# Optimization experiments

Hardware: AMD Instinct MI355X
Metric: run time of the kernel (lower is better)

Reference implementation:

```python
import jax, jax.numpy as jnp
import numpy as np
import math

B, S, D = 2, 2048, 1024
H, KV, HD = 16, 4, 64
N_REP = H // KV
ROPE_THETA = 1.0e6


def _rope_tables(seq_len, head_dim, theta):
    inv_freq = 1.0 / (theta ** (np.arange(0, head_dim, 2, dtype=np.float32) / head_dim))
    t = np.arange(seq_len, dtype=np.float32)
    freqs = np.outer(t, inv_freq)                      # [S, HD/2]
    emb = np.concatenate([freqs, freqs], axis=-1)      # [S, HD]
    return jnp.asarray(np.cos(emb)), jnp.asarray(np.sin(emb))


def setup_inputs() -> dict:
    key = jax.random.key(0)
    ks = jax.random.split(key, 6)
    cos, sin = _rope_tables(S, HD, ROPE_THETA)
    scale = 0.02
    return {
        "x": jax.random.normal(ks[0], (B, S, D), dtype=jnp.float32),
        "cos": cos,
        "sin": sin,
        "Wq": jax.random.normal(ks[1], (D, H * HD), dtype=jnp.float32) * scale,
        "Wk": jax.random.normal(ks[2], (D, KV * HD), dtype=jnp.float32) * scale,
        "Wv": jax.random.normal(ks[3], (D, KV * HD), dtype=jnp.float32) * scale,
        "Wo": jax.random.normal(ks[4], (H * HD, D), dtype=jnp.float32) * scale,
    }


def _rotate_half(u):
    u1, u2 = u[..., : HD // 2], u[..., HD // 2 :]
    return jnp.concatenate([-u2, u1], axis=-1)


def reference(x, cos, sin, Wq, Wk, Wv, Wo):
    bsz, seq_len, _ = x.shape
    q = (x @ Wq).reshape(bsz, seq_len, H, HD)   # [B,S,H,HD]
    k = (x @ Wk).reshape(bsz, seq_len, KV, HD)  # [B,S,KV,HD]
    v = (x @ Wv).reshape(bsz, seq_len, KV, HD)

    # RoPE: cos/sin [S,HD] broadcast over batch and heads (unsqueeze_dim=1)
    c = cos[:seq_len][None, :, None, :]
    s = sin[:seq_len][None, :, None, :]
    q = q * c + _rotate_half(q) * s
    k = k * c + _rotate_half(k) * s

    # repeat_kv: expand KV heads groupwise to H heads
    k = jnp.repeat(k, N_REP, axis=2)  # [B,S,H,HD]
    v = jnp.repeat(v, N_REP, axis=2)

    q = q.transpose(0, 2, 1, 3)  # [B,H,S,HD]
    k = k.transpose(0, 2, 1, 3)
    v = v.transpose(0, 2, 1, 3)

    scores = jnp.einsum("bhqd,bhkd->bhqk", q, k) / math.sqrt(HD)
    causal = jnp.tril(jnp.ones((seq_len, seq_len), dtype=bool))
    scores = jnp.where(causal[None, None], scores, jnp.finfo(jnp.float32).min)
    probs = jax.nn.softmax(scores.astype(jnp.float32), axis=-1).astype(x.dtype)

    out = jnp.einsum("bhqk,bhkd->bhqd", probs, v)        # [B,H,S,HD]
    out = out.transpose(0, 2, 1, 3).reshape(bsz, seq_len, H * HD)
    return out @ Wo
```

## Files before the change

kernel.cpp:

```cpp
#include <hip/hip_runtime.h>

#define SS 2048
#define NH 16
#define NKV 4
#define HD 64

typedef __bf16 bf16;
typedef __bf16 bf16x4 __attribute__((ext_vector_type(4)));
typedef __bf16 bf16x8 __attribute__((ext_vector_type(8)));
typedef float f32x4 __attribute__((ext_vector_type(4)));

#define SM_SCALE 0.18033688011f

__device__ __forceinline__ void gl_lds16(const bf16* g, bf16* l) {
    __builtin_amdgcn_global_load_lds((const __attribute__((address_space(1))) void*)g,
                                     (__attribute__((address_space(3))) void*)l, 16, 0, 0);
}

__global__ __launch_bounds__(256) void prep_kernel(
    const float* __restrict__ Wq, const float* __restrict__ Wk,
    const float* __restrict__ Wv, const float* __restrict__ Wo,
    bf16* __restrict__ wqkv_t, bf16* __restrict__ wo_t)
{
    const int blk = blockIdx.x;
    const int tid = threadIdx.x;
    const float* W; bf16* Wt; int N, n0, k0;
    if (blk < 256)      { W = Wq; Wt = wqkv_t;                       N = 1024; n0 = (blk & 15) * 64;         k0 = (blk >> 4) * 64; }
    else if (blk < 320) { W = Wk; Wt = wqkv_t + (size_t)1024 * 1024; N = 256;  n0 = ((blk - 256) & 3) * 64;  k0 = ((blk - 256) >> 2) * 64; }
    else if (blk < 384) { W = Wv; Wt = wqkv_t + (size_t)1280 * 1024; N = 256;  n0 = ((blk - 320) & 3) * 64;  k0 = ((blk - 320) >> 2) * 64; }
    else                { W = Wo; Wt = wo_t;                         N = 1024; n0 = ((blk - 384) & 15) * 64; k0 = ((blk - 384) >> 4) * 64; }

    __shared__ float Ts[64][65];
    const int c = tid & 63, rr = tid >> 6;
    #pragma unroll
    for (int i = 0; i < 16; ++i) {
        const int kk = i * 4 + rr;
        Ts[kk][c] = W[(size_t)(k0 + kk) * N + n0 + c];
    }
    __syncthreads();
    #pragma unroll
    for (int i = 0; i < 16; ++i) {
        const int nn = i * 4 + rr;
        Wt[(size_t)(n0 + nn) * 1024 + k0 + c] = (bf16)Ts[c][nn];
    }
}

template<int EPI>
__global__ __launch_bounds__(256) void gemm_bt_kernel(
    const bf16* __restrict__ A, const float* __restrict__ Af,
    const bf16* __restrict__ Bt, float* __restrict__ C,
    const float* __restrict__ cosp, const float* __restrict__ sinp,
    bf16* __restrict__ qo, bf16* __restrict__ ko, bf16* __restrict__ vto,
    int M, int N, int K)
{
    __shared__ bf16 As[128 * 64];
    __shared__ bf16 Bs[128 * 64];
    const int m0 = blockIdx.x * 128, n0 = blockIdx.y * 128;
    const int tid = threadIdx.x;
    const int w = tid >> 6, lane = tid & 63, g = lane >> 4, li = lane & 15;
    const int wm = w >> 1, wn = w & 1;

    f32x4 acc[4][4];
    const f32x4 z = {0.f, 0.f, 0.f, 0.f};
    #pragma unroll
    for (int i = 0; i < 4; ++i)
        #pragma unroll
        for (int j = 0; j < 4; ++j) acc[i][j] = z;

    const int srow = tid >> 3;
    const int schunk = ((tid & 7) ^ (srow & 7)) * 8;
    const bf16* pB[4];
    const bf16* pA[4];
    bf16* lB[4];
    bf16* lA[4];
    #pragma unroll
    for (int s = 0; s < 4; ++s) {
        pB[s] = Bt + (size_t)(n0 + s * 32 + srow) * K + schunk;
        lB[s] = Bs + s * 2048 + (size_t)w * 512;
        if (EPI == 0) pA[s] = A + (size_t)(m0 + s * 32 + srow) * K + schunk;
        lA[s] = As + s * 2048 + (size_t)w * 512;
    }

    for (int kk = 0; kk < K; kk += 64) {
        __syncthreads();
        if (EPI == 0) {
            #pragma unroll
            for (int s = 0; s < 4; ++s) gl_lds16(pA[s] + kk, lA[s]);
        } else {
            #pragma unroll
            for (int s = 0; s < 4; ++s) {
                const float* src = Af + (size_t)(m0 + s * 32 + srow) * K + kk + (tid & 7) * 8;
                const float4 v0 = *(const float4*)src;
                const float4 v1 = *(const float4*)(src + 4);
                bf16x8 t8;
                t8[0] = (bf16)v0.x; t8[1] = (bf16)v0.y; t8[2] = (bf16)v0.z; t8[3] = (bf16)v0.w;
                t8[4] = (bf16)v1.x; t8[5] = (bf16)v1.y; t8[6] = (bf16)v1.z; t8[7] = (bf16)v1.w;
                *(bf16x8*)&As[(s * 32 + srow) * 64 + schunk] = t8;
            }
        }
        #pragma unroll
        for (int s = 0; s < 4; ++s) gl_lds16(pB[s] + kk, lB[s]);
        __syncthreads();
        #pragma unroll
        for (int t = 0; t < 2; ++t) {
            const int phys = ((t * 4 + g) ^ (li & 7)) * 8;
            bf16x8 af[4], bfr[4];
            #pragma unroll
            for (int mi = 0; mi < 4; ++mi) af[mi] = *(const bf16x8*)&As[(wm * 64 + mi * 16 + li) * 64 + phys];
            #pragma unroll
            for (int ni = 0; ni < 4; ++ni) bfr[ni] = *(const bf16x8*)&Bs[(wn * 64 + ni * 16 + li) * 64 + phys];
            #pragma unroll
            for (int mi = 0; mi < 4; ++mi)
                #pragma unroll
                for (int ni = 0; ni < 4; ++ni)
                    acc[mi][ni] = __builtin_amdgcn_mfma_f32_16x16x32_bf16(af[mi], bfr[ni], acc[mi][ni], 0, 0, 0);
        }
    }

    const int row0 = m0 + wm * 64, col0 = n0 + wn * 64;
    if (EPI == 0) {
        #pragma unroll
        for (int mi = 0; mi < 4; ++mi)
            #pragma unroll
            for (int ni = 0; ni < 4; ++ni)
                #pragma unroll
                for (int r = 0; r < 4; ++r)
                    C[(size_t)(row0 + mi * 16 + g * 4 + r) * N + col0 + ni * 16 + li] = acc[mi][ni][r];
    } else {
        #pragma unroll
        for (int ni = 0; ni < 4; ++ni) {
            const int col = col0 + ni * 16 + li;
            const int d = col & 63;
            #pragma unroll
            for (int mi = 0; mi < 4; ++mi) {
                #pragma unroll
                for (int r = 0; r < 4; ++r) {
                    const int row = row0 + mi * 16 + g * 4 + r;
                    const int bb = row >> 11, s = row & 2047;
                    float val = acc[mi][ni][r];
                    if (col < 1280) {
                        const float pairv = acc[mi][ni ^ 2][r];
                        const float rot = (d < 32) ? -pairv : pairv;
                        val = val * cosp[s * 64 + d] + rot * sinp[s * 64 + d];
                    }
                    if (col < 1024) {
                        const int hh = col >> 6;
                        qo[(((size_t)bb * NH + hh) * SS + s) * HD + d] = (bf16)(val * SM_SCALE);
                    } else if (col < 1280) {
                        const int kh = (col - 1024) >> 6;
                        ko[(((size_t)bb * NKV + kh) * SS + s) * HD + d] = (bf16)val;
                    } else {
                        const int kh = (col - 1280) >> 6;
                        vto[(((size_t)bb * NKV + kh) * HD + d) * SS + s] = (bf16)val;
                    }
                }
            }
        }
    }
}

__global__ __launch_bounds__(256) void flash_kernel(const bf16* __restrict__ q, const bf16* __restrict__ k,
                                                    const bf16* __restrict__ vt, bf16* __restrict__ o)
{
    __shared__ bf16 Ks[128 * 64];
    __shared__ bf16 Vt[64 * 128];
    __shared__ bf16 Ps[4][16 * 64];

    const int blk = blockIdx.x;
    const int qt = 31 - (blk >> 5);
    const int h = blk & 15;
    const int b = (blk >> 4) & 1;
    const int kvh = h >> 2;
    const int tid = threadIdx.x;
    const int w = tid >> 6, lane = tid & 63, g = lane >> 4, li = lane & 15;

    const bf16* qh = q + ((size_t)b * NH + h) * SS * HD;
    const bf16* kh = k + ((size_t)b * NKV + kvh) * SS * HD;
    const bf16* vh = vt + ((size_t)b * NKV + kvh) * (size_t)HD * SS;

    bf16x8 ones;
    #pragma unroll
    for (int j = 0; j < 8; ++j) ones[j] = (bf16)1.0f;
    const f32x4 z = {0.f, 0.f, 0.f, 0.f};

    const bf16* qrow = qh + (size_t)(qt * 64 + w * 16 + li) * HD;
    bf16x8 qf[2];
    qf[0] = *(const bf16x8*)(qrow + g * 8);
    qf[1] = *(const bf16x8*)(qrow + 32 + g * 8);

    const int ksrow = tid >> 3;
    const int kchunk = ((tid & 7) ^ (ksrow & 7)) * 8;
    const int vsrow = tid >> 4;
    const int vchunk = (((tid & 15) ^ (vsrow & 7)) & 15) * 8;
    bf16* lK = Ks + (size_t)w * 512;
    bf16* lV = Vt + (size_t)w * 512;

    const int xm = (li & 7) << 1;

    f32x4 o_acc[4], l_acc;
    #pragma unroll
    for (int nt = 0; nt < 4; ++nt) o_acc[nt] = z;
    l_acc = z;

    for (int kt0 = 0; kt0 <= qt; kt0 += 2) {
        __syncthreads();
        {
            #pragma unroll
            for (int s = 0; s < 4; ++s)
                gl_lds16(kh + (size_t)(kt0 * 64 + s * 32 + ksrow) * HD + kchunk, lK + s * 2048);
            #pragma unroll
            for (int s = 0; s < 4; ++s)
                gl_lds16(vh + (size_t)(s * 16 + vsrow) * SS + kt0 * 64 + vchunk, lV + s * 2048);
        }
        __syncthreads();

        #pragma unroll
        for (int sub = 0; sub < 2; ++sub) {
            const int kt = kt0 + sub;
            if (kt > qt) break;

            f32x4 s_acc[4];
            #pragma unroll
            for (int nt = 0; nt < 4; ++nt) s_acc[nt] = z;
            #pragma unroll
            for (int t = 0; t < 2; ++t)
                #pragma unroll
                for (int nt = 0; nt < 4; ++nt) {
                    const bf16x8 kf = *(const bf16x8*)&Ks[(sub * 64 + nt * 16 + li) * 64 + (((t * 4 + g) ^ (li & 7)) * 8)];
                    s_acc[nt] = __builtin_amdgcn_mfma_f32_16x16x32_bf16(kf, qf[t], s_acc[nt], 0, 0, 0);
                }

            if (kt == qt) {
                const int qrow_in = w * 16 + li;
                #pragma unroll
                for (int nt = 0; nt < 4; ++nt) {
                    bf16x4 p4;
                    #pragma unroll
                    for (int r = 0; r < 4; ++r) {
                        float sv = s_acc[nt][r];
                        if (nt * 16 + g * 4 + r > qrow_in) sv = -1e30f;
                        p4[r] = (bf16)exp2f(sv);
                    }
                    *(bf16x4*)&Ps[w][li * 64 + (((nt * 4 + g) ^ xm) * 4)] = p4;
                }
            } else {
                #pragma unroll
                for (int nt = 0; nt < 4; ++nt) {
                    bf16x4 p4;
                    #pragma unroll
                    for (int r = 0; r < 4; ++r) p4[r] = (bf16)exp2f(s_acc[nt][r]);
                    *(bf16x4*)&Ps[w][li * 64 + (((nt * 4 + g) ^ xm) * 4)] = p4;
                }
            }

            #pragma unroll
            for (int t = 0; t < 2; ++t) {
                const bf16x8 pf = *(const bf16x8*)&Ps[w][li * 64 + (((t * 8 + g * 2) ^ xm) * 4)];
                l_acc = __builtin_amdgcn_mfma_f32_16x16x32_bf16(pf, ones, l_acc, 0, 0, 0);
                #pragma unroll
                for (int nt = 0; nt < 4; ++nt) {
                    const bf16x8 vf = *(const bf16x8*)&Vt[(nt * 16 + li) * 128 + (((sub * 8 + t * 4 + g) ^ (li & 7)) * 8)];
                    o_acc[nt] = __builtin_amdgcn_mfma_f32_16x16x32_bf16(pf, vf, o_acc[nt], 0, 0, 0);
                }
            }
        }
    }

    #pragma unroll
    for (int r = 0; r < 4; ++r) {
        const float inv = 1.f / l_acc[r];
        const int s = qt * 64 + w * 16 + g * 4 + r;
        bf16* orow = o + (((size_t)b * SS + s) * NH + h) * HD;
        #pragma unroll
        for (int nt = 0; nt < 4; ++nt) orow[nt * 16 + li] = (bf16)(o_acc[nt][r] * inv);
    }
}

extern "C" void kernel_launch(void* const* d_in, const int* in_sizes, int n_in,
                              void* d_out, int out_size, void* d_ws, size_t ws_size,
                              hipStream_t stream) {
    const float* x     = (const float*)d_in[0];
    const float* cos_t = (const float*)d_in[1];
    const float* sin_t = (const float*)d_in[2];
    const float* Wq    = (const float*)d_in[3];
    const float* Wk    = (const float*)d_in[4];
    const float* Wv    = (const float*)d_in[5];
    const float* Wo    = (const float*)d_in[6];
    float* out = (float*)d_out;

    char* wsb = (char*)d_ws;
    bf16* o_b    = (bf16*)(wsb);
    bf16* wqkv_t = (bf16*)(wsb + 8388608);
    bf16* wo_t   = (bf16*)(wsb + 11534336);
    bf16* q_b    = (bf16*)(wsb + 13631488);
    bf16* k_b    = (bf16*)(wsb + 22020096);
    bf16* vt_b   = (bf16*)(wsb + 24117248);

    prep_kernel<<<640, 256, 0, stream>>>(Wq, Wk, Wv, Wo, wqkv_t, wo_t);

    gemm_bt_kernel<2><<<dim3(32, 12), 256, 0, stream>>>(nullptr, x, wqkv_t, nullptr, cos_t, sin_t,
                                                        q_b, k_b, vt_b, 4096, 1536, 1024);
    flash_kernel<<<1024, 256, 0, stream>>>(q_b, k_b, vt_b, o_b);
    gemm_bt_kernel<0><<<dim3(32, 8), 256, 0, stream>>>(o_b, nullptr, wo_t, out, nullptr, nullptr,
                                                       nullptr, nullptr, nullptr, 4096, 1024, 1024);
}
```

Measured before the change: 184.1 us.

## Double-buffer GEMM LDS tiles and halve M tile to raise block count

Both GEMMs now use two LDS buffers per operand, prefetching the next K tile (including the fp32 activation loads for the QKV projection, converted after the MFMA loop) while the current tile is computed. The M tile shrinks from 128 to 64 rows, doubling the grids to 768 and 512 blocks so more of the 256 CUs have work. This trades lower per-block arithmetic intensity and more B-tile reloads for better latency hiding and occupancy.

```diff
diff --git a/kernel.cpp b/kernel.cpp
--- a/kernel.cpp
+++ b/kernel.cpp
@@ -53,74 +53,104 @@
     bf16* __restrict__ qo, bf16* __restrict__ ko, bf16* __restrict__ vto,
     int M, int N, int K)
 {
-    __shared__ bf16 As[128 * 64];
-    __shared__ bf16 Bs[128 * 64];
-    const int m0 = blockIdx.x * 128, n0 = blockIdx.y * 128;
+    __shared__ bf16 As[2][64 * 64];
+    __shared__ bf16 Bs[2][128 * 64];
+    const int m0 = blockIdx.x * 64, n0 = blockIdx.y * 128;
     const int tid = threadIdx.x;
     const int w = tid >> 6, lane = tid & 63, g = lane >> 4, li = lane & 15;
     const int wm = w >> 1, wn = w & 1;
 
-    f32x4 acc[4][4];
+    f32x4 acc[2][4];
     const f32x4 z = {0.f, 0.f, 0.f, 0.f};
     #pragma unroll
-    for (int i = 0; i < 4; ++i)
+    for (int i = 0; i < 2; ++i)
         #pragma unroll
         for (int j = 0; j < 4; ++j) acc[i][j] = z;
 
     const int srow = tid >> 3;
     const int schunk = ((tid & 7) ^ (srow & 7)) * 8;
-    const bf16* pB[4];
-    const bf16* pA[4];
-    bf16* lB[4];
-    bf16* lA[4];
-    #pragma unroll
-    for (int s = 0; s < 4; ++s) {
-        pB[s] = Bt + (size_t)(n0 + s * 32 + srow) * K + schunk;
-        lB[s] = Bs + s * 2048 + (size_t)w * 512;
-        if (EPI == 0) pA[s] = A + (size_t)(m0 + s * 32 + srow) * K + schunk;
-        lA[s] = As + s * 2048 + (size_t)w * 512;
-    }
-
-    for (int kk = 0; kk < K; kk += 64) {
-        __syncthreads();
-        if (EPI == 0) {
-            #pragma unroll
-            for (int s = 0; s < 4; ++s) gl_lds16(pA[s] + kk, lA[s]);
-        } else {
-            #pragma unroll
-            for (int s = 0; s < 4; ++s) {
-                const float* src = Af + (size_t)(m0 + s * 32 + srow) * K + kk + (tid & 7) * 8;
-                const float4 v0 = *(const float4*)src;
-                const float4 v1 = *(const float4*)(src + 4);
-                bf16x8 t8;
-                t8[0] = (bf16)v0.x; t8[1] = (bf16)v0.y; t8[2] = (bf16)v0.z; t8[3] = (bf16)v0.w;
-                t8[4] = (bf16)v1.x; t8[5] = (bf16)v1.y; t8[6] = (bf16)v1.z; t8[7] = (bf16)v1.w;
-                *(bf16x8*)&As[(s * 32 + srow) * 64 + schunk] = t8;
-            }
-        }
-        #pragma unroll
-        for (int s = 0; s < 4; ++s) gl_lds16(pB[s] + kk, lB[s]);
-        __syncthreads();
-        #pragma unroll
-        for (int t = 0; t < 2; ++t) {
-            const int phys = ((t * 4 + g) ^ (li & 7)) * 8;
-            bf16x8 af[4], bfr[4];
-            #pragma unroll
-            for (int mi = 0; mi < 4; ++mi) af[mi] = *(const bf16x8*)&As[(wm * 64 + mi * 16 + li) * 64 + phys];
-            #pragma unroll
-            for (int ni = 0; ni < 4; ++ni) bfr[ni] = *(const bf16x8*)&Bs[(wn * 64 + ni * 16 + li) * 64 + phys];
-            #pragma unroll
-            for (int mi = 0; mi < 4; ++mi)
+    const bf16* pB0 = Bt + (size_t)(n0 + srow) * K + schunk;
+    const bf16* pB1 = Bt + (size_t)(n0 + 32 + srow) * K + schunk;
+    const bf16* pB2 = Bt + (size_t)(n0 + 64 + srow) * K + schunk;
+    const bf16* pB3 = Bt + (size_t)(n0 + 96 + srow) * K + schunk;
+    const bf16* pA0 = (EPI == 0) ? A + (size_t)(m0 + srow) * K + schunk : nullptr;
+    const bf16* pA1 = (EPI == 0) ? A + (size_t)(m0 + 32 + srow) * K + schunk : nullptr;
+    const int lw = w * 512;
+
+    const int NT = K >> 6;
+
+    if (EPI == 0) {
+        gl_lds16(pA0, &As[0][lw]);
+        gl_lds16(pA1, &As[0][2048 + lw]);
+    } else {
+        #pragma unroll
+        for (int s = 0; s < 2; ++s) {
+            const float* src = Af + (size_t)(m0 + s * 32 + srow) * K + (tid & 7) * 8;
+            const float4 v0 = *(const float4*)src;
+            const float4 v1 = *(const float4*)(src + 4);
+            bf16x8 t8;
+            t8[0] = (bf16)v0.x; t8[1] = (bf16)v0.y; t8[2] = (bf16)v0.z; t8[3] = (bf16)v0.w;
+            t8[4] = (bf16)v1.x; t8[5] = (bf16)v1.y; t8[6] = (bf16)v1.z; t8[7] = (bf16)v1.w;
+            *(bf16x8*)&As[0][(s * 32 + srow) * 64 + schunk] = t8;
+        }
+    }
+    gl_lds16(pB0, &Bs[0][lw]);
+    gl_lds16(pB1, &Bs[0][2048 + lw]);
+    gl_lds16(pB2, &Bs[0][4096 + lw]);
+    gl_lds16(pB3, &Bs[0][6144 + lw]);
+    __syncthreads();
+
+    for (int t = 0; t < NT; ++t) {
+        const int cur = t & 1;
+        const int kk = (t + 1) << 6;
+        float4 va[2][2];
+        if (t + 1 < NT) {
+            if (EPI == 0) {
+                gl_lds16(pA0 + kk, &As[cur ^ 1][lw]);
+                gl_lds16(pA1 + kk, &As[cur ^ 1][2048 + lw]);
+            } else {
+                #pragma unroll
+                for (int s = 0; s < 2; ++s) {
+                    const float* src = Af + (size_t)(m0 + s * 32 + srow) * K + kk + (tid & 7) * 8;
+                    va[s][0] = *(const float4*)src;
+                    va[s][1] = *(const float4*)(src + 4);
+                }
+            }
+            gl_lds16(pB0 + kk, &Bs[cur ^ 1][lw]);
+            gl_lds16(pB1 + kk, &Bs[cur ^ 1][2048 + lw]);
+            gl_lds16(pB2 + kk, &Bs[cur ^ 1][4096 + lw]);
+            gl_lds16(pB3 + kk, &Bs[cur ^ 1][6144 + lw]);
+        }
+        #pragma unroll
+        for (int tt = 0; tt < 2; ++tt) {
+            const int phys = ((tt * 4 + g) ^ (li & 7)) * 8;
+            bf16x8 af[2], bfr[4];
+            #pragma unroll
+            for (int mi = 0; mi < 2; ++mi) af[mi] = *(const bf16x8*)&As[cur][(wm * 32 + mi * 16 + li) * 64 + phys];
+            #pragma unroll
+            for (int ni = 0; ni < 4; ++ni) bfr[ni] = *(const bf16x8*)&Bs[cur][(wn * 64 + ni * 16 + li) * 64 + phys];
+            #pragma unroll
+            for (int mi = 0; mi < 2; ++mi)
                 #pragma unroll
                 for (int ni = 0; ni < 4; ++ni)
                     acc[mi][ni] = __builtin_amdgcn_mfma_f32_16x16x32_bf16(af[mi], bfr[ni], acc[mi][ni], 0, 0, 0);
         }
-    }
-
-    const int row0 = m0 + wm * 64, col0 = n0 + wn * 64;
+        if (EPI == 2 && t + 1 < NT) {
+            #pragma unroll
+            for (int s = 0; s < 2; ++s) {
+                bf16x8 t8;
+                t8[0] = (bf16)va[s][0].x; t8[1] = (bf16)va[s][0].y; t8[2] = (bf16)va[s][0].z; t8[3] = (bf16)va[s][0].w;
+                t8[4] = (bf16)va[s][1].x; t8[5] = (bf16)va[s][1].y; t8[6] = (bf16)va[s][1].z; t8[7] = (bf16)va[s][1].w;
+                *(bf16x8*)&As[cur ^ 1][(s * 32 + srow) * 64 + schunk] = t8;
+            }
+        }
+        __syncthreads();
+    }
+
+    const int row0 = m0 + wm * 32, col0 = n0 + wn * 64;
     if (EPI == 0) {
         #pragma unroll
-        for (int mi = 0; mi < 4; ++mi)
+        for (int mi = 0; mi < 2; ++mi)
             #pragma unroll
             for (int ni = 0; ni < 4; ++ni)
                 #pragma unroll
@@ -132,7 +162,7 @@
             const int col = col0 + ni * 16 + li;
             const int d = col & 63;
             #pragma unroll
-            for (int mi = 0; mi < 4; ++mi) {
+            for (int mi = 0; mi < 2; ++mi) {
                 #pragma unroll
                 for (int r = 0; r < 4; ++r) {
                     const int row = row0 + mi * 16 + g * 4 + r;
@@ -298,9 +328,9 @@
 
     prep_kernel<<<640, 256, 0, stream>>>(Wq, Wk, Wv, Wo, wqkv_t, wo_t);
 
-    gemm_bt_kernel<2><<<dim3(32, 12), 256, 0, stream>>>(nullptr, x, wqkv_t, nullptr, cos_t, sin_t,
+    gemm_bt_kernel<2><<<dim3(64, 12), 256, 0, stream>>>(nullptr, x, wqkv_t, nullptr, cos_t, sin_t,
                                                         q_b, k_b, vt_b, 4096, 1536, 1024);
     flash_kernel<<<1024, 256, 0, stream>>>(q_b, k_b, vt_b, o_b);
-    gemm_bt_kernel<0><<<dim3(32, 8), 256, 0, stream>>>(o_b, nullptr, wo_t, out, nullptr, nullptr,
+    gemm_bt_kernel<0><<<dim3(64, 8), 256, 0, stream>>>(o_b, nullptr, wo_t, out, nullptr, nullptr,
                                                        nullptr, nullptr, nullptr, 4096, 1024, 1024);
 }
```

After: 166.9 us. 9.4% less time.

## Pre-convert x to bf16, double-buffer GEMM LDS tiles, remap blocks for L2 reuse

Applied to the files above, without the earlier changes.

The fp32-to-bf16 conversion of x moves into the prep kernel as extra blocks, so the QKV GEMM can load A straight into LDS with async global_load_lds like the output projection. The GEMM main loop becomes double-buffered: the next K tile is issued into the alternate LDS buffer while MFMAs run on the current one, with one barrier per iteration instead of two. Blocks are launched on a 1D grid remapped so groups of 8 row-blocks share column tiles, aiming for better L2 reuse. The cost is a round trip of x through a workspace buffer and twice the GEMM LDS footprint, which may lower occupancy.

```diff
diff --git a/kernel.cpp b/kernel.cpp
--- a/kernel.cpp
+++ b/kernel.cpp
@@ -18,12 +18,25 @@
 }
 
 __global__ __launch_bounds__(256) void prep_kernel(
+    const float* __restrict__ x,
     const float* __restrict__ Wq, const float* __restrict__ Wk,
     const float* __restrict__ Wv, const float* __restrict__ Wo,
-    bf16* __restrict__ wqkv_t, bf16* __restrict__ wo_t)
+    bf16* __restrict__ wqkv_t, bf16* __restrict__ wo_t, bf16* __restrict__ xb)
 {
     const int blk = blockIdx.x;
     const int tid = threadIdx.x;
+    if (blk >= 640) {
+        const size_t i0 = (size_t)(blk - 640) * 16384;
+        #pragma unroll
+        for (int i = 0; i < 16; ++i) {
+            const size_t idx = i0 + i * 1024 + tid * 4;
+            const float4 v = *(const float4*)&x[idx];
+            bf16x4 o4;
+            o4[0] = (bf16)v.x; o4[1] = (bf16)v.y; o4[2] = (bf16)v.z; o4[3] = (bf16)v.w;
+            *(bf16x4*)&xb[idx] = o4;
+        }
+        return;
+    }
     const float* W; bf16* Wt; int N, n0, k0;
     if (blk < 256)      { W = Wq; Wt = wqkv_t;                       N = 1024; n0 = (blk & 15) * 64;         k0 = (blk >> 4) * 64; }
     else if (blk < 320) { W = Wk; Wt = wqkv_t + (size_t)1024 * 1024; N = 256;  n0 = ((blk - 256) & 3) * 64;  k0 = ((blk - 256) >> 2) * 64; }
@@ -47,15 +60,18 @@
 
 template<int EPI>
 __global__ __launch_bounds__(256) void gemm_bt_kernel(
-    const bf16* __restrict__ A, const float* __restrict__ Af,
-    const bf16* __restrict__ Bt, float* __restrict__ C,
+    const bf16* __restrict__ A, const bf16* __restrict__ Bt, float* __restrict__ C,
     const float* __restrict__ cosp, const float* __restrict__ sinp,
     bf16* __restrict__ qo, bf16* __restrict__ ko, bf16* __restrict__ vto,
-    int M, int N, int K)
+    int N, int K, int CB)
 {
-    __shared__ bf16 As[128 * 64];
-    __shared__ bf16 Bs[128 * 64];
-    const int m0 = blockIdx.x * 128, n0 = blockIdx.y * 128;
+    __shared__ bf16 As[2][128 * 64];
+    __shared__ bf16 Bs[2][128 * 64];
+    const int bid = blockIdx.x;
+    const int j = bid >> 3;
+    const int rb = (bid & 7) + 8 * (j / CB);
+    const int cb = j % CB;
+    const int m0 = rb * 128, n0 = cb * 128;
     const int tid = threadIdx.x;
     const int w = tid >> 6, lane = tid & 63, g = lane >> 4, li = lane & 15;
     const int wm = w >> 1, wn = w & 1;
@@ -65,56 +81,51 @@
     #pragma unroll
     for (int i = 0; i < 4; ++i)
         #pragma unroll
-        for (int j = 0; j < 4; ++j) acc[i][j] = z;
+        for (int jj = 0; jj < 4; ++jj) acc[i][jj] = z;
 
     const int srow = tid >> 3;
     const int schunk = ((tid & 7) ^ (srow & 7)) * 8;
+    const bf16* pA[4];
     const bf16* pB[4];
-    const bf16* pA[4];
-    bf16* lB[4];
-    bf16* lA[4];
     #pragma unroll
     for (int s = 0; s < 4; ++s) {
+        pA[s] = A  + (size_t)(m0 + s * 32 + srow) * K + schunk;
         pB[s] = Bt + (size_t)(n0 + s * 32 + srow) * K + schunk;
-        lB[s] = Bs + s * 2048 + (size_t)w * 512;
-        if (EPI == 0) pA[s] = A + (size_t)(m0 + s * 32 + srow) * K + schunk;
-        lA[s] = As + s * 2048 + (size_t)w * 512;
-    }
-
-    for (int kk = 0; kk < K; kk += 64) {
-        __syncthreads();
-        if (EPI == 0) {
-            #pragma unroll
-            for (int s = 0; s < 4; ++s) gl_lds16(pA[s] + kk, lA[s]);
-        } else {
-            #pragma unroll
-            for (int s = 0; s < 4; ++s) {
-                const float* src = Af + (size_t)(m0 + s * 32 + srow) * K + kk + (tid & 7) * 8;
-                const float4 v0 = *(const float4*)src;
-                const float4 v1 = *(const float4*)(src + 4);
-                bf16x8 t8;
-                t8[0] = (bf16)v0.x; t8[1] = (bf16)v0.y; t8[2] = (bf16)v0.z; t8[3] = (bf16)v0.w;
-                t8[4] = (bf16)v1.x; t8[5] = (bf16)v1.y; t8[6] = (bf16)v1.z; t8[7] = (bf16)v1.w;
-                *(bf16x8*)&As[(s * 32 + srow) * 64 + schunk] = t8;
-            }
-        }
-        #pragma unroll
-        for (int s = 0; s < 4; ++s) gl_lds16(pB[s] + kk, lB[s]);
-        __syncthreads();
-        #pragma unroll
-        for (int t = 0; t < 2; ++t) {
-            const int phys = ((t * 4 + g) ^ (li & 7)) * 8;
+    }
+    const int lw = w * 512;
+
+    const int NT = K >> 6;
+
+    #pragma unroll
+    for (int s = 0; s < 4; ++s) gl_lds16(pA[s], &As[0][s * 2048 + lw]);
+    #pragma unroll
+    for (int s = 0; s < 4; ++s) gl_lds16(pB[s], &Bs[0][s * 2048 + lw]);
+    __syncthreads();
+
+    for (int t = 0; t < NT; ++t) {
+        const int cur = t & 1;
+        const int kk = (t + 1) << 6;
+        if (t + 1 < NT) {
+            #pragma unroll
+            for (int s = 0; s < 4; ++s) gl_lds16(pA[s] + kk, &As[cur ^ 1][s * 2048 + lw]);
+            #pragma unroll
+            for (int s = 0; s < 4; ++s) gl_lds16(pB[s] + kk, &Bs[cur ^ 1][s * 2048 + lw]);
+        }
+        #pragma unroll
+        for (int tt = 0; tt < 2; ++tt) {
+            const int phys = ((tt * 4 + g) ^ (li & 7)) * 8;
             bf16x8 af[4], bfr[4];
             #pragma unroll
-            for (int mi = 0; mi < 4; ++mi) af[mi] = *(const bf16x8*)&As[(wm * 64 + mi * 16 + li) * 64 + phys];
-            #pragma unroll
-            for (int ni = 0; ni < 4; ++ni) bfr[ni] = *(const bf16x8*)&Bs[(wn * 64 + ni * 16 + li) * 64 + phys];
+            for (int mi = 0; mi < 4; ++mi) af[mi] = *(const bf16x8*)&As[cur][(wm * 64 + mi * 16 + li) * 64 + phys];
+            #pragma unroll
+            for (int ni = 0; ni < 4; ++ni) bfr[ni] = *(const bf16x8*)&Bs[cur][(wn * 64 + ni * 16 + li) * 64 + phys];
             #pragma unroll
             for (int mi = 0; mi < 4; ++mi)
                 #pragma unroll
                 for (int ni = 0; ni < 4; ++ni)
                     acc[mi][ni] = __builtin_amdgcn_mfma_f32_16x16x32_bf16(af[mi], bfr[ni], acc[mi][ni], 0, 0, 0);
         }
+        __syncthreads();
     }
 
     const int row0 = m0 + wm * 64, col0 = n0 + wn * 64;
@@ -180,7 +191,7 @@
 
     bf16x8 ones;
     #pragma unroll
-    for (int j = 0; j < 8; ++j) ones[j] = (bf16)1.0f;
+    for (int jj = 0; jj < 8; ++jj) ones[jj] = (bf16)1.0f;
     const f32x4 z = {0.f, 0.f, 0.f, 0.f};
 
     const bf16* qrow = qh + (size_t)(qt * 64 + w * 16 + li) * HD;
@@ -295,12 +306,13 @@
     bf16* q_b    = (bf16*)(wsb + 13631488);
     bf16* k_b    = (bf16*)(wsb + 22020096);
     bf16* vt_b   = (bf16*)(wsb + 24117248);
-
-    prep_kernel<<<640, 256, 0, stream>>>(Wq, Wk, Wv, Wo, wqkv_t, wo_t);
-
-    gemm_bt_kernel<2><<<dim3(32, 12), 256, 0, stream>>>(nullptr, x, wqkv_t, nullptr, cos_t, sin_t,
-                                                        q_b, k_b, vt_b, 4096, 1536, 1024);
+    bf16* x_b    = (bf16*)(wsb + 26214400);
+
+    prep_kernel<<<896, 256, 0, stream>>>(x, Wq, Wk, Wv, Wo, wqkv_t, wo_t, x_b);
+
+    gemm_bt_kernel<2><<<384, 256, 0, stream>>>(x_b, wqkv_t, nullptr, cos_t, sin_t,
+                                               q_b, k_b, vt_b, 1536, 1024, 12);
     flash_kernel<<<1024, 256, 0, stream>>>(q_b, k_b, vt_b, o_b);
-    gemm_bt_kernel<0><<<dim3(32, 8), 256, 0, stream>>>(o_b, nullptr, wo_t, out, nullptr, nullptr,
-                                                       nullptr, nullptr, nullptr, 4096, 1024, 1024);
-}
+    gemm_bt_kernel<0><<<256, 256, 0, stream>>>(o_b, wo_t, out, nullptr, nullptr,
+                                               nullptr, nullptr, nullptr, 1024, 1024, 8);
+}
```

New measurement: 177.2 us. 1.04x faster.
